# Kernel optimization log

Measured on AMD Instinct MI355X. Metric: run time of the kernel, lower is better.

## Reference

```python
import jax, jax.numpy as jnp
import numpy as np

# ---- static config (mirrors init_kwargs) ----
EMBED_DIM = 128
NUM_HEADS = 4
N_SUB = 16       # token grid is N_SUB x N_SUB, seq = N_SUB**2
WINDOW = 4
SHIFT = 2
EPS = 1e-5
NEG_INF = -1e9


def _swin_mask(n_sub, ws, shift):
    """Standard Swin attention mask for shifted windows. [NW, T, T]."""
    img = np.zeros((n_sub, n_sub), np.int32)
    cnt = 0
    for hs in (slice(0, -ws), slice(-ws, -shift), slice(-shift, None)):
        for wsl in (slice(0, -ws), slice(-ws, -shift), slice(-shift, None)):
            img[hs, wsl] = cnt
            cnt += 1
    nw = n_sub // ws
    ids = img.reshape(nw, ws, nw, ws).transpose(0, 2, 1, 3).reshape(nw * nw, ws * ws)
    mask = np.where(ids[:, None, :] != ids[:, :, None], NEG_INF, 0.0).astype(np.float32)
    return jnp.asarray(mask)


MASK = _swin_mask(N_SUB, WINDOW, SHIFT)


def _inorm(v):
    # InstanceNorm2d (affine=False) over spatial dims, per (batch, seq, channel)
    m = v.mean(axis=(-2, -1), keepdims=True)
    var = v.var(axis=(-2, -1), keepdims=True)
    return (v - m) * jax.lax.rsqrt(var + EPS)


def _pw(x, w, b):
    # pointwise (1x1) linear over channel dim of [..., C, H, W]
    return jnp.einsum('...chw,cd->...dhw', x, w) + b[:, None, None]


def _window(x, nw, ws):
    # [B, n_sub, n_sub, C, H, W] -> [B, nw*nw, ws*ws, C, H, W]
    B = x.shape[0]
    C, H, W = x.shape[3:]
    x = x.reshape(B, nw, ws, nw, ws, C, H, W)
    return x.transpose(0, 1, 3, 2, 4, 5, 6, 7).reshape(B, nw * nw, ws * ws, C, H, W)


def _unwindow(x, nw, ws):
    B = x.shape[0]
    C, H, W = x.shape[3:]
    x = x.reshape(B, nw, nw, ws, ws, C, H, W)
    return x.transpose(0, 1, 3, 2, 4, 5, 6, 7).reshape(B, nw * ws, nw * ws, C, H, W)


def _swin_func_attn(v, w_q, b_q, w_k, b_k, w_v, b_v, w_o, b_o):
    B, S, C, H, W = v.shape
    nw = N_SUB // WINDOW
    g = v.reshape(B, N_SUB, N_SUB, C, H, W)
    if SHIFT > 0:
        g = jnp.roll(g, (-SHIFT, -SHIFT), axis=(1, 2))
    q = _window(_pw(g, w_q, b_q), nw, WINDOW)
    k = _window(_pw(g, w_k, b_k), nw, WINDOW)
    val = _window(_pw(g, w_v, b_v), nw, WINDOW)
    d = C // NUM_HEADS
    T = WINDOW * WINDOW
    split = lambda x: x.reshape(B, nw * nw, T, NUM_HEADS, d, H, W)
    q, k, val = split(q), split(k), split(val)
    # integral score: spatial mean of per-head dot products, scaled by sqrt(d)
    scale = 1.0 / (np.sqrt(d) * H * W)
    scores = jnp.einsum('bnthdxy,bnshdxy->bnhts', q, k) * scale
    scores = scores + MASK[None, :, None, :, :]
    attn = jax.nn.softmax(scores, axis=-1)
    o = jnp.einsum('bnhts,bnshdxy->bnthdxy', attn, val)
    o = o.reshape(B, nw * nw, T, C, H, W)
    o = _pw(o, w_o, b_o)
    o = _unwindow(o, nw, WINDOW)
    if SHIFT > 0:
        o = jnp.roll(o, (SHIFT, SHIFT), axis=(1, 2))
    return o.reshape(B, S, C, H, W)


def _mlp(x, w1, b1, w2, b2):
    return _pw(jax.nn.gelu(_pw(x, w1, b1)), w2, b2)


def setup_inputs() -> dict:
    key = jax.random.key(0)
    ks = jax.random.split(key, 8)
    B, S, C, H, W = 8, N_SUB * N_SUB, EMBED_DIM, 16, 16
    p = 0.02
    return {
        'v': jax.random.normal(ks[0], (B, S, C, H, W), jnp.float32),
        'w_q': jax.random.normal(ks[1], (C, C), jnp.float32) * p,
        'b_q': jnp.zeros((C,), jnp.float32),
        'w_k': jax.random.normal(ks[2], (C, C), jnp.float32) * p,
        'b_k': jnp.zeros((C,), jnp.float32),
        'w_v': jax.random.normal(ks[3], (C, C), jnp.float32) * p,
        'b_v': jnp.zeros((C,), jnp.float32),
        'w_o': jax.random.normal(ks[4], (C, C), jnp.float32) * p,
        'b_o': jnp.zeros((C,), jnp.float32),
        'w1': jax.random.normal(ks[5], (C, C), jnp.float32) * p,
        'b1': jnp.zeros((C,), jnp.float32),
        'w2': jax.random.normal(ks[6], (C, C), jnp.float32) * p,
        'b2': jnp.zeros((C,), jnp.float32),
    }


def reference(v, w_q, b_q, w_k, b_k, w_v, b_v, w_o, b_o, w1, b1, w2, b2):
    v = _swin_func_attn(_inorm(v), w_q, b_q, w_k, b_k, w_v, b_v, w_o, b_o) + v
    v = _mlp(_inorm(v), w1, b1, w2, b2) + v
    return v
```

## Files before the change

kernel.cpp:

```cpp
#include <hip/hip_runtime.h>
#include <cstdint>
#include <cstddef>

#define DI __device__ __forceinline__

typedef unsigned short u16;
typedef u16 u16x8 __attribute__((ext_vector_type(8)));
typedef u16 u16x4 __attribute__((ext_vector_type(4)));
typedef float f32x4 __attribute__((ext_vector_type(4)));
typedef __bf16 bf16x8 __attribute__((ext_vector_type(8)));

constexpr float EPSf  = 1e-5f;
constexpr float SCALE = 1.0f / (5.656854249492381f * 256.0f);

DI float bf2f(u16 u) { union { uint32_t i; float f; } v; v.i = ((uint32_t)u) << 16; return v.f; }
DI u16 f2bf(float f) {
    union { float f; uint32_t i; } v; v.f = f;
    uint32_t r = v.i + 0x7fffu + ((v.i >> 16) & 1u);
    return (u16)(r >> 16);
}

DI f32x4 MFMA(bf16x8 a, bf16x8 b, f32x4 c) {
    return __builtin_amdgcn_mfma_f32_16x16x32_bf16(a, b, c, 0, 0, 0);
}

DI int region3(int x) { return x < 12 ? 0 : (x < 14 ? 1 : 2); }

DI float gelu_f(float x) {
    float u = 1.5957691216f * x * (1.f + 0.044715f * x * x);
    return x * __builtin_amdgcn_rcpf(1.f + __expf(-u));
}

__global__ __launch_bounds__(256) void kw_prep(
        const float* __restrict__ w_q, const float* __restrict__ w_k,
        const float* __restrict__ w_v, const float* __restrict__ w_o,
        const float* __restrict__ w1,  const float* __restrict__ w2,
        u16* __restrict__ wt) {
    __shared__ float lds[128 * 129];
    const float* W;
    switch (blockIdx.x) {
        case 0: W = w_q; break; case 1: W = w_k; break; case 2: W = w_v; break;
        case 3: W = w_o; break; case 4: W = w1;  break; default: W = w2;  break;
    }
    u16* O = wt + blockIdx.x * 16384;
    int tid = threadIdx.x;
    for (int i = 0; i < 16; i++) {
        int flat = i * 1024 + tid * 4;
        float4 vv = *(const float4*)(W + flat);
        int c = flat >> 7, d = flat & 127;
        lds[c * 129 + d + 0] = vv.x; lds[c * 129 + d + 1] = vv.y;
        lds[c * 129 + d + 2] = vv.z; lds[c * 129 + d + 3] = vv.w;
    }
    __syncthreads();
    for (int i = 0; i < 32; i++) {
        int flat2 = i * 512 + tid * 2;
        int d = flat2 >> 7, c = flat2 & 127;
        u16 a = f2bf(lds[c * 129 + d]);
        u16 b = f2bf(lds[(c + 1) * 129 + d]);
        uint32_t pk = (uint32_t)a | ((uint32_t)b << 16);
        *(uint32_t*)(O + flat2) = pk;
    }
}

__global__ __launch_bounds__(512) void k2_qkv(
        const float* __restrict__ v, const u16* __restrict__ wt,
        const float* __restrict__ b_q, const float* __restrict__ b_k,
        const float* __restrict__ b_v,
        u16* __restrict__ Qg, u16* __restrict__ Kg, u16* __restrict__ Vg) {
    __shared__ u16 Abuf[256 * 136];
    __shared__ float red[2][4][128];
    __shared__ float stats[2][128];

    int tid = threadIdx.x;
    int wtk = blockIdx.x;
    int b = wtk >> 8, n = (wtk >> 4) & 15, t = wtk & 15;
    int wi = n >> 2, wj = n & 3, ti = t >> 2, tj = t & 3;
    int si = (wi * 4 + ti + 2) & 15, sj = (wj * 4 + tj + 2) & 15;
    const float* src = v + (size_t)(b * 256 + si * 16 + sj) * 32768;

    int xy = tid & 255, chh = tid >> 8;
    #pragma unroll 4
    for (int g = 0; g < 16; g++) {
        int c0 = chh * 64 + g * 4;
        float x0 = src[(c0 + 0) * 256 + xy];
        float x1 = src[(c0 + 1) * 256 + xy];
        float x2 = src[(c0 + 2) * 256 + xy];
        float x3 = src[(c0 + 3) * 256 + xy];
        u16x4 u; u.x = f2bf(x0); u.y = f2bf(x1); u.z = f2bf(x2); u.w = f2bf(x3);
        *(u16x4*)&Abuf[xy * 136 + c0] = u;
    }
    __syncthreads();
    {
        int c = tid & 127, p = tid >> 7;
        float s = 0.f, q = 0.f;
        for (int k = 0; k < 64; k++) {
            float x = bf2f(Abuf[(p * 64 + k) * 136 + c]);
            s += x; q += x * x;
        }
        red[0][p][c] = s; red[1][p][c] = q;
    }
    __syncthreads();
    if (tid < 128) {
        int c = tid;
        float s = red[0][0][c] + red[0][1][c] + red[0][2][c] + red[0][3][c];
        float q = red[1][0][c] + red[1][1][c] + red[1][2][c] + red[1][3][c];
        float mean = s * (1.f / 256.f);
        float var = q * (1.f / 256.f) - mean * mean;
        stats[0][c] = mean; stats[1][c] = rsqrtf(var + EPSf);
    }
    __syncthreads();
    for (int g = 0; g < 16; g++) {
        int c0 = chh * 64 + g * 4;
        u16x4 u = *(u16x4*)&Abuf[xy * 136 + c0];
        u.x = f2bf((bf2f(u.x) - stats[0][c0 + 0]) * stats[1][c0 + 0]);
        u.y = f2bf((bf2f(u.y) - stats[0][c0 + 1]) * stats[1][c0 + 1]);
        u.z = f2bf((bf2f(u.z) - stats[0][c0 + 2]) * stats[1][c0 + 2]);
        u.w = f2bf((bf2f(u.w) - stats[0][c0 + 3]) * stats[1][c0 + 3]);
        *(u16x4*)&Abuf[xy * 136 + c0] = u;
    }
    __syncthreads();

    int wave = tid >> 6, lane = tid & 63;
    int lrow = lane & 15, quad = lane >> 4;
    bf16x8 afr[2][4];
    for (int mi = 0; mi < 2; mi++) {
        int mt = wave * 2 + mi;
        for (int kt = 0; kt < 4; kt++)
            afr[mi][kt] = *(const bf16x8*)&Abuf[(mt * 16 + lrow) * 136 + kt * 32 + quad * 8];
    }
    __syncthreads();
    u16* WTs  = Abuf;
    u16* stgw = Abuf + 17408 + wave * 2176;
    for (int w = 0; w < 3; w++) {
        const u16* WTp = wt + w * 16384;
        const float* bias = (w == 0) ? b_q : (w == 1) ? b_k : b_v;
        u16* O = ((w == 0) ? Qg : (w == 1) ? Kg : Vg) + (size_t)wtk * 32768;
        if (w) __syncthreads();
        for (int i = 0; i < 4; i++) {
            int flat = i * 4096 + tid * 8;
            *(u16x8*)&WTs[(flat >> 7) * 136 + (flat & 127)] =
                *(const u16x8*)&WTp[flat];
        }
        __syncthreads();
        f32x4 acc[2][8];
        for (int mi = 0; mi < 2; mi++)
            for (int nt = 0; nt < 8; nt++) acc[mi][nt] = (f32x4){0.f, 0.f, 0.f, 0.f};
        for (int kt = 0; kt < 4; kt++) {
            for (int nt = 0; nt < 8; nt++) {
                bf16x8 bfr = *(const bf16x8*)&WTs[(nt * 16 + lrow) * 136 + kt * 32 + quad * 8];
                acc[0][nt] = MFMA(afr[0][kt], bfr, acc[0][nt]);
                acc[1][nt] = MFMA(afr[1][kt], bfr, acc[1][nt]);
            }
        }
        for (int mi = 0; mi < 2; mi++) {
            int mt = wave * 2 + mi;
            for (int nt = 0; nt < 8; nt++) {
                int d = nt * 16 + lrow;
                float bv = bias[d];
                for (int r = 0; r < 4; r++)
                    stgw[(quad * 4 + r) * 136 + d] = f2bf(acc[mi][nt][r] + bv);
            }
            for (int ro = 0; ro < 4; ro++) {
                int flat = ro * 512 + lane * 8;
                *(u16x8*)&O[mt * 2048 + flat] =
                    *(const u16x8*)&stgw[(flat >> 7) * 136 + (flat & 127)];
            }
        }
    }
}

__global__ __launch_bounds__(1024, 4) void k3_scores(
        const u16* __restrict__ Qg, const u16* __restrict__ Kg,
        float* __restrict__ spart) {
    __shared__ f32x4 red3[3][4][64];
    int tid = threadIdx.x;
    int bid = blockIdx.x;
    int b = bid >> 5, n = (bid >> 1) & 15, half = bid & 1;
    int wtb = (b * 16 + n) * 16;
    int lane = tid & 63, wave = tid >> 6;
    int head = wave & 3, sub = wave >> 2;
    int lrow = lane & 15, quad = lane >> 4;
    int xyb = half * 128 + sub * 32;
    const u16* Qp = Qg + (size_t)(wtb + lrow) * 32768 + (size_t)xyb * 128 + head * 32 + quad * 8;
    const u16* Kp = Kg + (size_t)(wtb + lrow) * 32768 + (size_t)xyb * 128 + head * 32 + quad * 8;
    f32x4 acc = {0.f, 0.f, 0.f, 0.f};
    #pragma unroll 4
    for (int kt = 0; kt < 32; kt++) {
        bf16x8 aq = *(const bf16x8*)(Qp + kt * 128);
        bf16x8 bk = *(const bf16x8*)(Kp + kt * 128);
        acc = MFMA(aq, bk, acc);
    }
    if (sub) red3[sub - 1][head][lane] = acc;
    __syncthreads();
    if (sub == 0) {
        f32x4 a0 = red3[0][head][lane];
        f32x4 a1 = red3[1][head][lane];
        f32x4 a2 = red3[2][head][lane];
        acc = acc + a0 + a1 + a2;
        float* sp = spart + (size_t)(((half * 8 + b) * 16 + n) * 4 + head) * 256;
        for (int r = 0; r < 4; r++) sp[(quad * 4 + r) * 16 + lrow] = acc[r];
    }
}

__global__ __launch_bounds__(512) void k4_attnout(
        const float* __restrict__ v, const u16* __restrict__ Vg,
        const float* __restrict__ spart, const u16* __restrict__ wt,
        const float* __restrict__ b_o, u16* __restrict__ v2) {
    __shared__ u16 Vc[32768];
    __shared__ u16 Obuf[256 * 136];
    __shared__ float attn[4][16][16];
    int tid = threadIdx.x;
    int bid = blockIdx.x;
    int b = bid >> 6, n = (bid >> 2) & 15, qtr = bid & 3;
    int wi = n >> 2, wj = n & 3;
    int wtb = (b * 16 + n) * 16;

    if (tid < 64) {
        int h = tid >> 4, t = tid & 15;
        int it = wi * 4 + (t >> 2) , jt = wj * 4 + (t & 3);
        int rt = region3(it) * 3 + region3(jt);
        const float* sp0 = spart + (size_t)(((0 + b) * 16 + n) * 4 + h) * 256 + t * 16;
        const float* sp1 = spart + (size_t)(((8 + b) * 16 + n) * 4 + h) * 256 + t * 16;
        float vals[16]; float mx = -1e30f;
        for (int s = 0; s < 16; s++) {
            int is = wi * 4 + (s >> 2), js = wj * 4 + (s & 3);
            int rs = region3(is) * 3 + region3(js);
            float sc = (sp0[s] + sp1[s]) * SCALE + (rs == rt ? 0.f : -1e9f);
            vals[s] = sc; mx = fmaxf(mx, sc);
        }
        float sum = 0.f;
        for (int s = 0; s < 16; s++) { vals[s] = __expf(vals[s] - mx); sum += vals[s]; }
        float inv = 1.f / sum;
        for (int s = 0; s < 16; s++) attn[h][t][s] = vals[s] * inv;
    }
    __syncthreads();

    int lane = tid & 63, wave = tid >> 6;
    int lrow = lane & 15, quad = lane >> 4;
    const u16* WoT = wt + 3 * 16384;

    for (int sub = 0; sub < 4; sub++) {
        int xyb = qtr * 64 + sub * 16;
        if (sub) __syncthreads();
        for (int it = 0; it < 8; it++) {
            int flat = (it * 512 + tid) * 8;
            int s = flat >> 11, rem = flat & 2047;
            *(u16x8*)&Vc[flat] =
                *(const u16x8*)&Vg[(size_t)(wtb + s) * 32768 + xyb * 128 + rem];
        }
        __syncthreads();
        {
            int c = tid & 127, xg = tid >> 7;
            int h = c >> 5;
            float vreg[4][16];
            for (int rep = 0; rep < 4; rep++) {
                int xyl = xg * 4 + rep;
                for (int s = 0; s < 16; s++)
                    vreg[rep][s] = bf2f(Vc[s * 2048 + xyl * 128 + c]);
            }
            for (int t = 0; t < 16; t++) {
                float oa0 = 0.f, oa1 = 0.f, oa2 = 0.f, oa3 = 0.f;
                for (int s = 0; s < 16; s++) {
                    float a = attn[h][t][s];
                    oa0 += a * vreg[0][s]; oa1 += a * vreg[1][s];
                    oa2 += a * vreg[2][s]; oa3 += a * vreg[3][s];
                }
                Obuf[(t * 16 + xg * 4 + 0) * 136 + c] = f2bf(oa0);
                Obuf[(t * 16 + xg * 4 + 1) * 136 + c] = f2bf(oa1);
                Obuf[(t * 16 + xg * 4 + 2) * 136 + c] = f2bf(oa2);
                Obuf[(t * 16 + xg * 4 + 3) * 136 + c] = f2bf(oa3);
            }
        }
        __syncthreads();
        bf16x8 afr[2][4];
        for (int mi = 0; mi < 2; mi++) {
            int mt = wave * 2 + mi;
            for (int kt = 0; kt < 4; kt++)
                afr[mi][kt] = *(const bf16x8*)&Obuf[(mt * 16 + lrow) * 136 + kt * 32 + quad * 8];
        }
        f32x4 acc[2][8];
        for (int mi = 0; mi < 2; mi++)
            for (int nt = 0; nt < 8; nt++) acc[mi][nt] = (f32x4){0.f, 0.f, 0.f, 0.f};
        for (int kt = 0; kt < 4; kt++) {
            for (int nt = 0; nt < 8; nt++) {
                bf16x8 bfr = *(const bf16x8*)&WoT[(nt * 16 + lrow) * 128 + kt * 32 + quad * 8];
                acc[0][nt] = MFMA(afr[0][kt], bfr, acc[0][nt]);
                acc[1][nt] = MFMA(afr[1][kt], bfr, acc[1][nt]);
            }
        }
        u16* stgw = Vc + wave * 2176;
        for (int mi = 0; mi < 2; mi++) {
            int mt = wave * 2 + mi;
            int sd = (((wi * 4 + (mt >> 2) + 2) & 15) << 4) | ((wj * 4 + (mt & 3) + 2) & 15);
            size_t tokbase = (size_t)(b * 256 + sd) * 32768;
            for (int nt = 0; nt < 8; nt++) {
                int c = nt * 16 + lrow;
                float bv = b_o[c];
                float4 res = *(const float4*)&v[tokbase + (size_t)c * 256 + xyb + quad * 4];
                stgw[(quad * 4 + 0) * 136 + c] = f2bf(acc[mi][nt][0] + bv + res.x);
                stgw[(quad * 4 + 1) * 136 + c] = f2bf(acc[mi][nt][1] + bv + res.y);
                stgw[(quad * 4 + 2) * 136 + c] = f2bf(acc[mi][nt][2] + bv + res.z);
                stgw[(quad * 4 + 3) * 136 + c] = f2bf(acc[mi][nt][3] + bv + res.w);
            }
            size_t obase = tokbase + (size_t)xyb * 128;
            for (int ro = 0; ro < 4; ro++) {
                int flat = ro * 512 + lane * 8;
                *(u16x8*)&v2[obase + flat] =
                    *(const u16x8*)&stgw[(flat >> 7) * 136 + (flat & 127)];
            }
        }
    }
}

__global__ __launch_bounds__(512) void k6_mlp(
        const u16* __restrict__ v2, const u16* __restrict__ wt,
        const float* __restrict__ b1, const float* __restrict__ b2,
        float* __restrict__ out) {
    __shared__ u16 Nbuf[256 * 136];
    __shared__ u16 Hbuf[256 * 136];
    __shared__ float red[2][4][128];
    __shared__ float stats[3][128];
    int tid = threadIdx.x;
    size_t tok = blockIdx.x;
    const u16* src = v2 + tok * 32768;

    for (int it = 0; it < 8; it++) {
        int flat = (it * 512 + tid) * 8;
        int xy = flat >> 7, c = flat & 127;
        *(u16x8*)&Nbuf[xy * 136 + c] = *(const u16x8*)&src[flat];
    }
    __syncthreads();
    {
        int c = tid & 127, p = tid >> 7;
        float s = 0.f, q = 0.f;
        for (int k = 0; k < 64; k++) {
            float x = bf2f(Nbuf[(p * 64 + k) * 136 + c]);
            s += x; q += x * x;
        }
        red[0][p][c] = s; red[1][p][c] = q;
    }
    __syncthreads();
    if (tid < 128) {
        int c = tid;
        float s = red[0][0][c] + red[0][1][c] + red[0][2][c] + red[0][3][c];
        float q = red[1][0][c] + red[1][1][c] + red[1][2][c] + red[1][3][c];
        float mean = s * (1.f / 256.f);
        float var = q * (1.f / 256.f) - mean * mean;
        float rstd = rsqrtf(var + EPSf);
        stats[0][c] = mean; stats[1][c] = rstd; stats[2][c] = (var + EPSf) * rstd;
    }
    __syncthreads();
    {
        int c0 = (tid & 31) * 4, xyB = tid >> 5;
        for (int g = 0; g < 16; g++) {
            int xy = g * 16 + xyB;
            u16x4 u = *(u16x4*)&Nbuf[xy * 136 + c0];
            u.x = f2bf((bf2f(u.x) - stats[0][c0 + 0]) * stats[1][c0 + 0]);
            u.y = f2bf((bf2f(u.y) - stats[0][c0 + 1]) * stats[1][c0 + 1]);
            u.z = f2bf((bf2f(u.z) - stats[0][c0 + 2]) * stats[1][c0 + 2]);
            u.w = f2bf((bf2f(u.w) - stats[0][c0 + 3]) * stats[1][c0 + 3]);
            *(u16x4*)&Nbuf[xy * 136 + c0] = u;
        }
    }
    {
        const u16* W1T = wt + 4 * 16384;
        for (int i = 0; i < 4; i++) {
            int flat = i * 4096 + tid * 8;
            *(u16x8*)&Hbuf[(flat >> 7) * 136 + (flat & 127)] = *(const u16x8*)&W1T[flat];
        }
    }
    __syncthreads();

    int wave = tid >> 6, lane = tid & 63;
    int lrow = lane & 15, quad = lane >> 4;
    const u16* W2T = wt + 5 * 16384;

    {
        bf16x8 afr[2][4];
        for (int mi = 0; mi < 2; mi++) {
            int mt = wave * 2 + mi;
            for (int kt = 0; kt < 4; kt++)
                afr[mi][kt] = *(const bf16x8*)&Nbuf[(mt * 16 + lrow) * 136 + kt * 32 + quad * 8];
        }
        f32x4 acc[2][8];
        for (int mi = 0; mi < 2; mi++)
            for (int nt = 0; nt < 8; nt++) acc[mi][nt] = (f32x4){0.f, 0.f, 0.f, 0.f};
        for (int kt = 0; kt < 4; kt++) {
            for (int nt = 0; nt < 8; nt++) {
                bf16x8 bfr = *(const bf16x8*)&Hbuf[(nt * 16 + lrow) * 136 + kt * 32 + quad * 8];
                acc[0][nt] = MFMA(afr[0][kt], bfr, acc[0][nt]);
                acc[1][nt] = MFMA(afr[1][kt], bfr, acc[1][nt]);
            }
        }
        __syncthreads();
        for (int mi = 0; mi < 2; mi++) {
            int mt = wave * 2 + mi;
            for (int nt = 0; nt < 8; nt++) {
                int c = nt * 16 + lrow;
                float bv = b1[c];
                for (int r = 0; r < 4; r++) {
                    float x = acc[mi][nt][r] + bv;
                    Hbuf[(mt * 16 + quad * 4 + r) * 136 + c] = f2bf(gelu_f(x));
                }
            }
        }
    }
    {
        bf16x8 afr[2][4];
        for (int mi = 0; mi < 2; mi++) {
            int mt = wave * 2 + mi;
            for (int kt = 0; kt < 4; kt++)
                afr[mi][kt] = *(const bf16x8*)&Hbuf[(mt * 16 + lrow) * 136 + kt * 32 + quad * 8];
        }
        f32x4 acc[2][8];
        for (int mi = 0; mi < 2; mi++)
            for (int nt = 0; nt < 8; nt++) acc[mi][nt] = (f32x4){0.f, 0.f, 0.f, 0.f};
        for (int kt = 0; kt < 4; kt++) {
            for (int nt = 0; nt < 8; nt++) {
                bf16x8 bfr = *(const bf16x8*)&W2T[(nt * 16 + lrow) * 128 + kt * 32 + quad * 8];
                acc[0][nt] = MFMA(afr[0][kt], bfr, acc[0][nt]);
                acc[1][nt] = MFMA(afr[1][kt], bfr, acc[1][nt]);
            }
        }
        for (int mi = 0; mi < 2; mi++) {
            int mt = wave * 2 + mi;
            for (int nt = 0; nt < 8; nt++) {
                int c = nt * 16 + lrow;
                float mean = stats[0][c], sd = stats[2][c], bv = b2[c];
                f32x4 o4;
                for (int r = 0; r < 4; r++) {
                    int m = mt * 16 + quad * 4 + r;
                    float n2v = bf2f(Nbuf[m * 136 + c]);
                    o4[r] = acc[mi][nt][r] + bv + n2v * sd + mean;
                }
                *(f32x4*)&out[tok * 32768 + (size_t)c * 256 + mt * 16 + quad * 4] = o4;
            }
        }
    }
}

extern "C" void kernel_launch(void* const* d_in, const int* in_sizes, int n_in,
                              void* d_out, int out_size, void* d_ws, size_t ws_size,
                              hipStream_t stream) {
    const float* v   = (const float*)d_in[0];
    const float* w_q = (const float*)d_in[1];
    const float* b_q = (const float*)d_in[2];
    const float* w_k = (const float*)d_in[3];
    const float* b_k = (const float*)d_in[4];
    const float* w_v = (const float*)d_in[5];
    const float* b_v = (const float*)d_in[6];
    const float* w_o = (const float*)d_in[7];
    const float* b_o = (const float*)d_in[8];
    const float* w1  = (const float*)d_in[9];
    const float* b1  = (const float*)d_in[10];
    const float* w2  = (const float*)d_in[11];
    const float* b2  = (const float*)d_in[12];

    u16*   wt    = (u16*)d_ws;
    float* spart = (float*)((char*)d_ws + 196608);
    u16*   Qg    = (u16*)((char*)d_ws + 1245184);
    u16*   v2    = Qg;
    u16*   Vg    = (u16*)d_out;
    u16*   Kg    = (u16*)d_out + 67108864;
    float* out   = (float*)d_out;

    kw_prep  <<<6,    256,  0, stream>>>(w_q, w_k, w_v, w_o, w1, w2, wt);
    k2_qkv   <<<2048, 512,  0, stream>>>(v, wt, b_q, b_k, b_v, Qg, Kg, Vg);
    k3_scores<<<256,  1024, 0, stream>>>(Qg, Kg, spart);
    k4_attnout<<<512, 512,  0, stream>>>(v, Vg, spart, wt, b_o, v2);
    k6_mlp   <<<2048, 512,  0, stream>>>(v2, wt, b1, b2, out);
}
```

Baseline: 1.042 ms.

## Fuse instance-norm into MFMA fragment loads and keep attention output in registers

k2_qkv now loads the input with coalesced float4 reads into a channel-major LDS buffer, and applies the normalization as an FMA while building the MFMA A fragments. This removes a separate normalize pass and one LDS round-trip. k4_attnout computes the attention-weighted V directly into bf16 register fragments from an XOR-swizzled V tile, which drops the Obuf staging buffer and its LDS traffic. k6_mlp also fuses normalization into the fragment loads, overlaps the W1 load with the input load, and uses the raw stored value for the residual instead of reconstructing it from the normalized value. Launch bounds request four blocks per CU and loops are fully unrolled, which risks register pressure or spills.

```diff
diff --git a/kernel.cpp b/kernel.cpp
--- a/kernel.cpp
+++ b/kernel.cpp
@@ -19,6 +19,7 @@
     uint32_t r = v.i + 0x7fffu + ((v.i >> 16) & 1u);
     return (u16)(r >> 16);
 }
+DI bf16x8 u2b(u16x8 u) { union { u16x8 a; bf16x8 b; } v; v.a = u; return v.b; }
 
 DI f32x4 MFMA(bf16x8 a, bf16x8 b, f32x4 c) {
     return __builtin_amdgcn_mfma_f32_16x16x32_bf16(a, b, c, 0, 0, 0);
@@ -62,12 +63,12 @@
     }
 }
 
-__global__ __launch_bounds__(512) void k2_qkv(
+__global__ __launch_bounds__(512, 4) void k2_qkv(
         const float* __restrict__ v, const u16* __restrict__ wt,
         const float* __restrict__ b_q, const float* __restrict__ b_k,
         const float* __restrict__ b_v,
         u16* __restrict__ Qg, u16* __restrict__ Kg, u16* __restrict__ Vg) {
-    __shared__ u16 Abuf[256 * 136];
+    __shared__ __align__(16) u16 Raw[34816];
     __shared__ float red[2][4][128];
     __shared__ float stats[2][128];
 
@@ -78,24 +79,25 @@
     int si = (wi * 4 + ti + 2) & 15, sj = (wj * 4 + tj + 2) & 15;
     const float* src = v + (size_t)(b * 256 + si * 16 + sj) * 32768;
 
-    int xy = tid & 255, chh = tid >> 8;
-    #pragma unroll 4
-    for (int g = 0; g < 16; g++) {
-        int c0 = chh * 64 + g * 4;
-        float x0 = src[(c0 + 0) * 256 + xy];
-        float x1 = src[(c0 + 1) * 256 + xy];
-        float x2 = src[(c0 + 2) * 256 + xy];
-        float x3 = src[(c0 + 3) * 256 + xy];
-        u16x4 u; u.x = f2bf(x0); u.y = f2bf(x1); u.z = f2bf(x2); u.w = f2bf(x3);
-        *(u16x4*)&Abuf[xy * 136 + c0] = u;
+    int wave = tid >> 6, lane = tid & 63;
+
+    #pragma unroll
+    for (int i = 0; i < 16; i++) {
+        int c = i * 8 + wave;
+        float4 f = *(const float4*)(src + c * 256 + lane * 4);
+        u16x4 u; u.x = f2bf(f.x); u.y = f2bf(f.y); u.z = f2bf(f.z); u.w = f2bf(f.w);
+        *(u16x4*)&Raw[c * 268 + lane * 4] = u;
     }
     __syncthreads();
     {
         int c = tid & 127, p = tid >> 7;
         float s = 0.f, q = 0.f;
-        for (int k = 0; k < 64; k++) {
-            float x = bf2f(Abuf[(p * 64 + k) * 136 + c]);
-            s += x; q += x * x;
+        #pragma unroll
+        for (int k = 0; k < 16; k++) {
+            u16x4 u = *(const u16x4*)&Raw[c * 268 + p * 64 + k * 4];
+            float x0 = bf2f(u.x), x1 = bf2f(u.y), x2 = bf2f(u.z), x3 = bf2f(u.w);
+            s += x0 + x1 + x2 + x3;
+            q += x0 * x0 + x1 * x1 + x2 * x2 + x3 * x3;
         }
         red[0][p][c] = s; red[1][p][c] = q;
     }
@@ -106,36 +108,43 @@
         float q = red[1][0][c] + red[1][1][c] + red[1][2][c] + red[1][3][c];
         float mean = s * (1.f / 256.f);
         float var = q * (1.f / 256.f) - mean * mean;
-        stats[0][c] = mean; stats[1][c] = rsqrtf(var + EPSf);
-    }
-    __syncthreads();
-    for (int g = 0; g < 16; g++) {
-        int c0 = chh * 64 + g * 4;
-        u16x4 u = *(u16x4*)&Abuf[xy * 136 + c0];
-        u.x = f2bf((bf2f(u.x) - stats[0][c0 + 0]) * stats[1][c0 + 0]);
-        u.y = f2bf((bf2f(u.y) - stats[0][c0 + 1]) * stats[1][c0 + 1]);
-        u.z = f2bf((bf2f(u.z) - stats[0][c0 + 2]) * stats[1][c0 + 2]);
-        u.w = f2bf((bf2f(u.w) - stats[0][c0 + 3]) * stats[1][c0 + 3]);
-        *(u16x4*)&Abuf[xy * 136 + c0] = u;
-    }
-    __syncthreads();
-
-    int wave = tid >> 6, lane = tid & 63;
+        float a = rsqrtf(var + EPSf);
+        stats[0][c] = a; stats[1][c] = -mean * a;
+    }
+    __syncthreads();
+
     int lrow = lane & 15, quad = lane >> 4;
     bf16x8 afr[2][4];
-    for (int mi = 0; mi < 2; mi++) {
-        int mt = wave * 2 + mi;
-        for (int kt = 0; kt < 4; kt++)
-            afr[mi][kt] = *(const bf16x8*)&Abuf[(mt * 16 + lrow) * 136 + kt * 32 + quad * 8];
-    }
-    __syncthreads();
-    u16* WTs  = Abuf;
-    u16* stgw = Abuf + 17408 + wave * 2176;
+    #pragma unroll
+    for (int kt = 0; kt < 4; kt++) {
+        float sa[8], sb[8];
+        #pragma unroll
+        for (int j = 0; j < 8; j++) {
+            int c = kt * 32 + quad * 8 + j;
+            sa[j] = stats[0][c]; sb[j] = stats[1][c];
+        }
+        #pragma unroll
+        for (int mi = 0; mi < 2; mi++) {
+            int xy = (wave * 2 + mi) * 16 + lrow;
+            u16x8 o;
+            #pragma unroll
+            for (int j = 0; j < 8; j++) {
+                int c = kt * 32 + quad * 8 + j;
+                o[j] = f2bf(fmaf(bf2f(Raw[c * 268 + xy]), sa[j], sb[j]));
+            }
+            afr[mi][kt] = u2b(o);
+        }
+    }
+    __syncthreads();
+
+    u16* WTs  = Raw;
+    u16* stgw = Raw + 17408 + wave * 2176;
     for (int w = 0; w < 3; w++) {
         const u16* WTp = wt + w * 16384;
         const float* bias = (w == 0) ? b_q : (w == 1) ? b_k : b_v;
         u16* O = ((w == 0) ? Qg : (w == 1) ? Kg : Vg) + (size_t)wtk * 32768;
         if (w) __syncthreads();
+        #pragma unroll
         for (int i = 0; i < 4; i++) {
             int flat = i * 4096 + tid * 8;
             *(u16x8*)&WTs[(flat >> 7) * 136 + (flat & 127)] =
@@ -143,23 +152,31 @@
         }
         __syncthreads();
         f32x4 acc[2][8];
+        #pragma unroll
         for (int mi = 0; mi < 2; mi++)
+            #pragma unroll
             for (int nt = 0; nt < 8; nt++) acc[mi][nt] = (f32x4){0.f, 0.f, 0.f, 0.f};
+        #pragma unroll
         for (int kt = 0; kt < 4; kt++) {
+            #pragma unroll
             for (int nt = 0; nt < 8; nt++) {
                 bf16x8 bfr = *(const bf16x8*)&WTs[(nt * 16 + lrow) * 136 + kt * 32 + quad * 8];
                 acc[0][nt] = MFMA(afr[0][kt], bfr, acc[0][nt]);
                 acc[1][nt] = MFMA(afr[1][kt], bfr, acc[1][nt]);
             }
         }
+        #pragma unroll
         for (int mi = 0; mi < 2; mi++) {
             int mt = wave * 2 + mi;
+            #pragma unroll
             for (int nt = 0; nt < 8; nt++) {
                 int d = nt * 16 + lrow;
                 float bv = bias[d];
+                #pragma unroll
                 for (int r = 0; r < 4; r++)
                     stgw[(quad * 4 + r) * 136 + d] = f2bf(acc[mi][nt][r] + bv);
             }
+            #pragma unroll
             for (int ro = 0; ro < 4; ro++) {
                 int flat = ro * 512 + lane * 8;
                 *(u16x8*)&O[mt * 2048 + flat] =
@@ -202,12 +219,11 @@
     }
 }
 
-__global__ __launch_bounds__(512) void k4_attnout(
+__global__ __launch_bounds__(512, 4) void k4_attnout(
         const float* __restrict__ v, const u16* __restrict__ Vg,
         const float* __restrict__ spart, const u16* __restrict__ wt,
         const float* __restrict__ b_o, u16* __restrict__ v2) {
-    __shared__ u16 Vc[32768];
-    __shared__ u16 Obuf[256 * 136];
+    __shared__ __align__(16) u16 Vc[32768];
     __shared__ float attn[4][16][16];
     int tid = threadIdx.x;
     int bid = blockIdx.x;
@@ -242,67 +258,72 @@
     for (int sub = 0; sub < 4; sub++) {
         int xyb = qtr * 64 + sub * 16;
         if (sub) __syncthreads();
+        #pragma unroll
         for (int it = 0; it < 8; it++) {
             int flat = (it * 512 + tid) * 8;
             int s = flat >> 11, rem = flat & 2047;
-            *(u16x8*)&Vc[flat] =
+            int xyl = rem >> 7, ch = (rem & 127) >> 3;
+            *(u16x8*)&Vc[s * 2048 + xyl * 128 + ((ch ^ (xyl & 7)) << 3)] =
                 *(const u16x8*)&Vg[(size_t)(wtb + s) * 32768 + xyb * 128 + rem];
         }
         __syncthreads();
-        {
-            int c = tid & 127, xg = tid >> 7;
-            int h = c >> 5;
-            float vreg[4][16];
-            for (int rep = 0; rep < 4; rep++) {
-                int xyl = xg * 4 + rep;
-                for (int s = 0; s < 16; s++)
-                    vreg[rep][s] = bf2f(Vc[s * 2048 + xyl * 128 + c]);
-            }
-            for (int t = 0; t < 16; t++) {
-                float oa0 = 0.f, oa1 = 0.f, oa2 = 0.f, oa3 = 0.f;
-                for (int s = 0; s < 16; s++) {
-                    float a = attn[h][t][s];
-                    oa0 += a * vreg[0][s]; oa1 += a * vreg[1][s];
-                    oa2 += a * vreg[2][s]; oa3 += a * vreg[3][s];
+        bf16x8 pa[2][4];
+        int t0 = wave * 2, t1 = wave * 2 + 1;
+        #pragma unroll
+        for (int kt = 0; kt < 4; kt++) {
+            float oa[8], ob[8];
+            #pragma unroll
+            for (int j = 0; j < 8; j++) { oa[j] = 0.f; ob[j] = 0.f; }
+            #pragma unroll
+            for (int s = 0; s < 16; s++) {
+                float a0 = attn[kt][t0][s], a1 = attn[kt][t1][s];
+                u16x8 vv = *(const u16x8*)&Vc[s * 2048 + lrow * 128 +
+                                              (((kt * 4 + quad) ^ (lrow & 7)) << 3)];
+                #pragma unroll
+                for (int j = 0; j < 8; j++) {
+                    float x = bf2f(vv[j]);
+                    oa[j] = fmaf(a0, x, oa[j]);
+                    ob[j] = fmaf(a1, x, ob[j]);
                 }
-                Obuf[(t * 16 + xg * 4 + 0) * 136 + c] = f2bf(oa0);
-                Obuf[(t * 16 + xg * 4 + 1) * 136 + c] = f2bf(oa1);
-                Obuf[(t * 16 + xg * 4 + 2) * 136 + c] = f2bf(oa2);
-                Obuf[(t * 16 + xg * 4 + 3) * 136 + c] = f2bf(oa3);
-            }
+            }
+            u16x8 ua, ub;
+            #pragma unroll
+            for (int j = 0; j < 8; j++) { ua[j] = f2bf(oa[j]); ub[j] = f2bf(ob[j]); }
+            pa[0][kt] = u2b(ua); pa[1][kt] = u2b(ub);
         }
         __syncthreads();
-        bf16x8 afr[2][4];
-        for (int mi = 0; mi < 2; mi++) {
-            int mt = wave * 2 + mi;
-            for (int kt = 0; kt < 4; kt++)
-                afr[mi][kt] = *(const bf16x8*)&Obuf[(mt * 16 + lrow) * 136 + kt * 32 + quad * 8];
-        }
         f32x4 acc[2][8];
+        #pragma unroll
         for (int mi = 0; mi < 2; mi++)
+            #pragma unroll
             for (int nt = 0; nt < 8; nt++) acc[mi][nt] = (f32x4){0.f, 0.f, 0.f, 0.f};
+        #pragma unroll
         for (int kt = 0; kt < 4; kt++) {
+            #pragma unroll
             for (int nt = 0; nt < 8; nt++) {
                 bf16x8 bfr = *(const bf16x8*)&WoT[(nt * 16 + lrow) * 128 + kt * 32 + quad * 8];
-                acc[0][nt] = MFMA(afr[0][kt], bfr, acc[0][nt]);
-                acc[1][nt] = MFMA(afr[1][kt], bfr, acc[1][nt]);
+                acc[0][nt] = MFMA(pa[0][kt], bfr, acc[0][nt]);
+                acc[1][nt] = MFMA(pa[1][kt], bfr, acc[1][nt]);
             }
         }
         u16* stgw = Vc + wave * 2176;
+        #pragma unroll
         for (int mi = 0; mi < 2; mi++) {
             int mt = wave * 2 + mi;
             int sd = (((wi * 4 + (mt >> 2) + 2) & 15) << 4) | ((wj * 4 + (mt & 3) + 2) & 15);
             size_t tokbase = (size_t)(b * 256 + sd) * 32768;
-            for (int nt = 0; nt < 8; nt++) {
-                int c = nt * 16 + lrow;
-                float bv = b_o[c];
-                float4 res = *(const float4*)&v[tokbase + (size_t)c * 256 + xyb + quad * 4];
-                stgw[(quad * 4 + 0) * 136 + c] = f2bf(acc[mi][nt][0] + bv + res.x);
-                stgw[(quad * 4 + 1) * 136 + c] = f2bf(acc[mi][nt][1] + bv + res.y);
-                stgw[(quad * 4 + 2) * 136 + c] = f2bf(acc[mi][nt][2] + bv + res.z);
-                stgw[(quad * 4 + 3) * 136 + c] = f2bf(acc[mi][nt][3] + bv + res.w);
+            #pragma unroll
+            for (int nt = 0; nt < 8; nt++) {
+                int cc = nt * 16 + lrow;
+                float bv = b_o[cc];
+                float4 res = *(const float4*)&v[tokbase + (size_t)cc * 256 + xyb + quad * 4];
+                stgw[(quad * 4 + 0) * 136 + cc] = f2bf(acc[mi][nt][0] + bv + res.x);
+                stgw[(quad * 4 + 1) * 136 + cc] = f2bf(acc[mi][nt][1] + bv + res.y);
+                stgw[(quad * 4 + 2) * 136 + cc] = f2bf(acc[mi][nt][2] + bv + res.z);
+                stgw[(quad * 4 + 3) * 136 + cc] = f2bf(acc[mi][nt][3] + bv + res.w);
             }
             size_t obase = tokbase + (size_t)xyb * 128;
+            #pragma unroll
             for (int ro = 0; ro < 4; ro++) {
                 int flat = ro * 512 + lane * 8;
                 *(u16x8*)&v2[obase + flat] =
@@ -312,22 +333,31 @@
     }
 }
 
-__global__ __launch_bounds__(512) void k6_mlp(
+__global__ __launch_bounds__(512, 4) void k6_mlp(
         const u16* __restrict__ v2, const u16* __restrict__ wt,
         const float* __restrict__ b1, const float* __restrict__ b2,
         float* __restrict__ out) {
-    __shared__ u16 Nbuf[256 * 136];
-    __shared__ u16 Hbuf[256 * 136];
+    __shared__ __align__(16) u16 Nbuf[256 * 136];
+    __shared__ __align__(16) u16 Hbuf[256 * 136];
     __shared__ float red[2][4][128];
-    __shared__ float stats[3][128];
+    __shared__ float stats[2][128];
     int tid = threadIdx.x;
     size_t tok = blockIdx.x;
     const u16* src = v2 + tok * 32768;
 
+    #pragma unroll
     for (int it = 0; it < 8; it++) {
         int flat = (it * 512 + tid) * 8;
         int xy = flat >> 7, c = flat & 127;
         *(u16x8*)&Nbuf[xy * 136 + c] = *(const u16x8*)&src[flat];
+    }
+    {
+        const u16* W1T = wt + 4 * 16384;
+        #pragma unroll
+        for (int i = 0; i < 4; i++) {
+            int flat = i * 4096 + tid * 8;
+            *(u16x8*)&Hbuf[(flat >> 7) * 136 + (flat & 127)] = *(const u16x8*)&W1T[flat];
+        }
     }
     __syncthreads();
     {
@@ -346,28 +376,8 @@
         float q = red[1][0][c] + red[1][1][c] + red[1][2][c] + red[1][3][c];
         float mean = s * (1.f / 256.f);
         float var = q * (1.f / 256.f) - mean * mean;
-        float rstd = rsqrtf(var + EPSf);
-        stats[0][c] = mean; stats[1][c] = rstd; stats[2][c] = (var + EPSf) * rstd;
-    }
-    __syncthreads();
-    {
-        int c0 = (tid & 31) * 4, xyB = tid >> 5;
-        for (int g = 0; g < 16; g++) {
-            int xy = g * 16 + xyB;
-            u16x4 u = *(u16x4*)&Nbuf[xy * 136 + c0];
-            u.x = f2bf((bf2f(u.x) - stats[0][c0 + 0]) * stats[1][c0 + 0]);
-            u.y = f2bf((bf2f(u.y) - stats[0][c0 + 1]) * stats[1][c0 + 1]);
-            u.z = f2bf((bf2f(u.z) - stats[0][c0 + 2]) * stats[1][c0 + 2]);
-            u.w = f2bf((bf2f(u.w) - stats[0][c0 + 3]) * stats[1][c0 + 3]);
-            *(u16x4*)&Nbuf[xy * 136 + c0] = u;
-        }
-    }
-    {
-        const u16* W1T = wt + 4 * 16384;
-        for (int i = 0; i < 4; i++) {
-            int flat = i * 4096 + tid * 8;
-            *(u16x8*)&Hbuf[(flat >> 7) * 136 + (flat & 127)] = *(const u16x8*)&W1T[flat];
-        }
+        float a = rsqrtf(var + EPSf);
+        stats[0][c] = a; stats[1][c] = -mean * a;
     }
     __syncthreads();
 
@@ -377,15 +387,33 @@
 
     {
         bf16x8 afr[2][4];
-        for (int mi = 0; mi < 2; mi++) {
-            int mt = wave * 2 + mi;
-            for (int kt = 0; kt < 4; kt++)
-                afr[mi][kt] = *(const bf16x8*)&Nbuf[(mt * 16 + lrow) * 136 + kt * 32 + quad * 8];
+        #pragma unroll
+        for (int kt = 0; kt < 4; kt++) {
+            float sa[8], sb[8];
+            #pragma unroll
+            for (int j = 0; j < 8; j++) {
+                int c = kt * 32 + quad * 8 + j;
+                sa[j] = stats[0][c]; sb[j] = stats[1][c];
+            }
+            #pragma unroll
+            for (int mi = 0; mi < 2; mi++) {
+                int mt = wave * 2 + mi;
+                u16x8 raw = *(const u16x8*)&Nbuf[(mt * 16 + lrow) * 136 + kt * 32 + quad * 8];
+                u16x8 o;
+                #pragma unroll
+                for (int j = 0; j < 8; j++)
+                    o[j] = f2bf(fmaf(bf2f(raw[j]), sa[j], sb[j]));
+                afr[mi][kt] = u2b(o);
+            }
         }
         f32x4 acc[2][8];
+        #pragma unroll
         for (int mi = 0; mi < 2; mi++)
+            #pragma unroll
             for (int nt = 0; nt < 8; nt++) acc[mi][nt] = (f32x4){0.f, 0.f, 0.f, 0.f};
+        #pragma unroll
         for (int kt = 0; kt < 4; kt++) {
+            #pragma unroll
             for (int nt = 0; nt < 8; nt++) {
                 bf16x8 bfr = *(const bf16x8*)&Hbuf[(nt * 16 + lrow) * 136 + kt * 32 + quad * 8];
                 acc[0][nt] = MFMA(afr[0][kt], bfr, acc[0][nt]);
@@ -393,11 +421,14 @@
             }
         }
         __syncthreads();
+        #pragma unroll
         for (int mi = 0; mi < 2; mi++) {
             int mt = wave * 2 + mi;
+            #pragma unroll
             for (int nt = 0; nt < 8; nt++) {
                 int c = nt * 16 + lrow;
                 float bv = b1[c];
+                #pragma unroll
                 for (int r = 0; r < 4; r++) {
                     float x = acc[mi][nt][r] + bv;
                     Hbuf[(mt * 16 + quad * 4 + r) * 136 + c] = f2bf(gelu_f(x));
@@ -407,31 +438,39 @@
     }
     {
         bf16x8 afr[2][4];
+        #pragma unroll
         for (int mi = 0; mi < 2; mi++) {
             int mt = wave * 2 + mi;
+            #pragma unroll
             for (int kt = 0; kt < 4; kt++)
                 afr[mi][kt] = *(const bf16x8*)&Hbuf[(mt * 16 + lrow) * 136 + kt * 32 + quad * 8];
         }
         f32x4 acc[2][8];
+        #pragma unroll
         for (int mi = 0; mi < 2; mi++)
+            #pragma unroll
             for (int nt = 0; nt < 8; nt++) acc[mi][nt] = (f32x4){0.f, 0.f, 0.f, 0.f};
+        #pragma unroll
         for (int kt = 0; kt < 4; kt++) {
+            #pragma unroll
             for (int nt = 0; nt < 8; nt++) {
                 bf16x8 bfr = *(const bf16x8*)&W2T[(nt * 16 + lrow) * 128 + kt * 32 + quad * 8];
                 acc[0][nt] = MFMA(afr[0][kt], bfr, acc[0][nt]);
                 acc[1][nt] = MFMA(afr[1][kt], bfr, acc[1][nt]);
             }
         }
+        #pragma unroll
         for (int mi = 0; mi < 2; mi++) {
             int mt = wave * 2 + mi;
+            #pragma unroll
             for (int nt = 0; nt < 8; nt++) {
                 int c = nt * 16 + lrow;
-                float mean = stats[0][c], sd = stats[2][c], bv = b2[c];
+                float bv = b2[c];
                 f32x4 o4;
+                #pragma unroll
                 for (int r = 0; r < 4; r++) {
                     int m = mt * 16 + quad * 4 + r;
-                    float n2v = bf2f(Nbuf[m * 136 + c]);
-                    o4[r] = acc[mi][nt][r] + bv + n2v * sd + mean;
+                    o4[r] = acc[mi][nt][r] + bv + bf2f(Nbuf[m * 136 + c]);
                 }
                 *(f32x4*)&out[tok * 32768 + (size_t)c * 256 + mt * 16 + quad * 4] = o4;
             }
```

Result: slower. 1.232 ms (+18.3%).
